# Optimization experiments

Measured on AMD Instinct MI355X. Metric: run time of the kernel, lower is better.

## Reference

```python
import jax, jax.numpy as jnp
import numpy as np

LAYER_BS = 63
N_SITES = 12
B = 2048


def _kaiming_uniform(key, shape, fan_in):
    # torch kaiming_uniform_ with a=0: bound = sqrt(6/fan_in)
    bound = np.sqrt(6.0 / fan_in)
    return jax.random.uniform(key, shape, jnp.float32, -bound, bound)


def _cnn12(x, w):
    # x: (B, L, 12, Cin); w: (L, 3*Cin, Cout)
    nn0 = jnp.roll(x, -1, axis=-2) + jnp.roll(x, 3, axis=-2)
    nnn0 = jnp.roll(x, -2, axis=-2) + jnp.roll(x, 4, axis=-2)
    c0 = jnp.concatenate([nn0, nnn0], axis=-1)          # (B,L,12,2*Cin)
    c1 = c0 + jnp.roll(c0, -2, axis=-2)
    allc = jnp.concatenate([x, c1], axis=-1)            # (B,L,12,3*Cin)
    return jnp.einsum('blsc,lco->blso', allc, w)


def _batch_linear(x, w, b):
    # x: (B, L, F); w: (L, F, O); b: (L, O)
    return jnp.einsum('blf,lfo->blo', x, w) + b


def setup_inputs() -> dict:
    key = jax.random.key(0)
    ks = jax.random.split(key, 9)
    zs = jax.random.normal(ks[0], (B, LAYER_BS, N_SITES, 2), jnp.float32)
    # CNN weights: (L, 3*Cin, Cout); kaiming fan_in = 3*Cin
    w1 = _kaiming_uniform(ks[1], (LAYER_BS, 6, 32), 6)
    w2 = _kaiming_uniform(ks[2], (LAYER_BS, 96, 64), 96)
    fw1 = _kaiming_uniform(ks[3], (LAYER_BS, 128, 64), 128)
    fb1 = jax.random.uniform(ks[4], (LAYER_BS, 64), jnp.float32, -1 / np.sqrt(128), 1 / np.sqrt(128))
    fw2 = _kaiming_uniform(ks[5], (LAYER_BS, 64, 64), 64)
    fb2 = jax.random.uniform(ks[6], (LAYER_BS, 64), jnp.float32, -1 / np.sqrt(64), 1 / np.sqrt(64))
    fw3 = _kaiming_uniform(ks[7], (LAYER_BS, 64, 1), 64)
    fb3 = jax.random.uniform(ks[8], (LAYER_BS, 1), jnp.float32, -1 / np.sqrt(64), 1 / np.sqrt(64))
    return {"zs": zs, "w1": w1, "w2": w2, "fw1": fw1, "fb1": fb1,
            "fw2": fw2, "fb2": fb2, "fw3": fw3, "fb3": fb3}


def reference(zs, w1, w2, fw1, fb1, fw2, fb2, fw3, fb3):
    h = jax.nn.relu(_cnn12(zs, w1))                     # (B,L,12,32)
    h = jax.nn.relu(_cnn12(h, w2))                      # (B,L,12,64)
    h = jnp.concatenate([h.mean(axis=-2), h.max(axis=-2)], axis=-1)
    h = jax.nn.relu(_batch_linear(h, fw1, fb1))
    h = jax.nn.relu(_batch_linear(h, fw2, fb2))
    out = _batch_linear(h, fw3, fb3)                    # (B,L,1)
    return out[..., 0]                                  # (B,L)
```

## Files before the change

kernel.cpp:

```cpp
#include <hip/hip_runtime.h>


#define LNUM 63
#define BT 16
#define NBT 128
#define WSL 19968

typedef __attribute__((ext_vector_type(8))) _Float16 half8;
typedef __attribute__((ext_vector_type(2))) _Float16 half2v;
typedef __attribute__((ext_vector_type(4))) float floatx4;
typedef __attribute__((ext_vector_type(4))) unsigned uint4v;

static __device__ __forceinline__ unsigned cvtpk(float a, float b) {
    return __builtin_bit_cast(unsigned, __builtin_amdgcn_cvt_pkrtz(a, b));
}
static __device__ __forceinline__ half2v u2h(unsigned u) { return __builtin_bit_cast(half2v, u); }
static __device__ __forceinline__ float hlo16(unsigned short s) {
    return (float)__builtin_bit_cast(_Float16, s);
}
static __device__ __forceinline__ int w12(int v) { return v >= 12 ? v - 12 : v; }
static __device__ __forceinline__ float2 add2(float2 a, float2 b) { return make_float2(a.x + b.x, a.y + b.y); }

#define O_POOLDW 3072
#define O_POOLUS 6144
#define O_POOL2  0
#define O_G2     1280

__global__ void prep(const float* __restrict__ w2, const float* __restrict__ fw1,
                     const float* __restrict__ fw2, unsigned short* __restrict__ ws) {
    __shared__ float S[8192];
    const int l = blockIdx.x, r = blockIdx.y, t = threadIdx.x;
    if (r == 0) {
        const float4* src = (const float4*)(w2 + (size_t)l * 6144);
        #pragma unroll
        for (int j = 0; j < 6; ++j) *(float4*)(S + 4 * (t + 256 * j)) = src[t + 256 * j];
        __syncthreads();
        unsigned* dst = (unsigned*)(ws + (size_t)l * WSL);
        #pragma unroll
        for (int j = 0; j < 13; ++j) {
            int i = j * 256 + t, o = i / 52, cp = i - 52 * o, c = 2 * cp;
            dst[i] = cvtpk(S[c * 64 + o], S[c * 64 + 64 + o]);
        }
    } else if (r == 1) {
        const float4* src = (const float4*)(fw1 + (size_t)l * 8192);
        #pragma unroll
        for (int j = 0; j < 8; ++j) *(float4*)(S + 4 * (t + 256 * j)) = src[t + 256 * j];
        __syncthreads();
        unsigned* dst = (unsigned*)(ws + (size_t)l * WSL + 6656);
        #pragma unroll
        for (int j = 0; j < 17; ++j) {
            int i = j * 256 + t, o = i / 68, cp = i - 68 * o;
            dst[i] = cvtpk(S[cp * 64 + o], S[(64 + cp) * 64 + o]);
        }
    } else {
        const float4* src = (const float4*)(fw2 + (size_t)l * 4096);
        #pragma unroll
        for (int j = 0; j < 4; ++j) *(float4*)(S + 4 * (t + 256 * j)) = src[t + 256 * j];
        __syncthreads();
        unsigned* dst = (unsigned*)(ws + (size_t)l * WSL + 15360);
        #pragma unroll
        for (int j = 0; j < 9; ++j) {
            int i = j * 256 + t, o = i / 36, cp = i - 36 * o, c = 2 * cp;
            dst[i] = cvtpk(S[c * 64 + o], S[c * 64 + 64 + o]);
        }
    }
}

__global__ __launch_bounds__(256, 4) void fused_nn(
    const float* __restrict__ zs,  const float* __restrict__ w1,
    const float* __restrict__ fb1, const float* __restrict__ fb2,
    const float* __restrict__ fw3, const float* __restrict__ fb3,
    const unsigned short* __restrict__ ws,
    float* __restrict__ out)
{
    __shared__ __align__(16) unsigned U[4160];
    unsigned short* USH = (unsigned short*)U;

    const int t    = threadIdx.x;
    const int lane = t & 63;
    const int wv   = t >> 6;
    const int n    = lane & 15;
    const int quad = lane >> 4;
    const int l    = blockIdx.x / NBT;
    const int b0   = (blockIdx.x % NBT) * BT;

    uint4v bwp[3][4];
    {
        const uint4v* w2q = (const uint4v*)(ws + (size_t)l * WSL);
        #pragma unroll
        for (int ks = 0; ks < 3; ++ks)
            #pragma unroll
            for (int nt = 0; nt < 4; ++nt)
                bwp[ks][nt] = w2q[(nt * 16 + n) * 13 + ks * 4 + quad];
    }

    {
        const int b = t >> 4, cpair = t & 15, c0 = cpair * 2;
        const float* xb = zs + ((size_t)(b0 + b) * LNUM + l) * 24;
        float4 xq[6];
        #pragma unroll
        for (int q = 0; q < 6; ++q) xq[q] = *(const float4*)(xb + q * 4);
        float2 xv[12], xr[12], xA[12], xB[12];
        #pragma unroll
        for (int s = 0; s < 12; ++s)
            xv[s] = (s & 1) ? make_float2(xq[s >> 1].z, xq[s >> 1].w)
                            : make_float2(xq[s >> 1].x, xq[s >> 1].y);
        #pragma unroll
        for (int s = 0; s < 12; ++s) xr[s] = add2(xv[w12(s + 1)], xv[w12(s + 11)]);
        #pragma unroll
        for (int s = 0; s < 12; ++s) {
            xA[s] = add2(xr[w12(s + 2)], xr[w12(s + 10)]);
            xB[s] = add2(xr[w12(s + 3)], xr[w12(s + 9)]);
        }
        const float* wl = w1 + (size_t)l * 192 + c0;
        const float2 w0  = *(const float2*)(wl);
        const float2 w1v = *(const float2*)(wl + 32);
        const float2 w2v = *(const float2*)(wl + 64);
        const float2 w3v = *(const float2*)(wl + 96);
        const float2 w4v = *(const float2*)(wl + 128);
        const float2 w5v = *(const float2*)(wl + 160);
        #pragma unroll
        for (int s = 0; s < 12; ++s) {
            float hx = xv[s].x*w0.x + xv[s].y*w1v.x + xA[s].x*w2v.x + xA[s].y*w3v.x
                     + xB[s].x*w4v.x + xB[s].y*w5v.x;
            float hy = xv[s].x*w0.y + xv[s].y*w1v.y + xA[s].x*w2v.y + xA[s].y*w3v.y
                     + xB[s].x*w4v.y + xB[s].y*w5v.y;
            U[(b * 12 + s) * 20 + cpair] = cvtpk(fmaxf(hx, 0.f), fmaxf(hy, 0.f));
        }
    }
    const float bias1 = fb1[(size_t)l * 64 + wv * 16 + n];
    const float bias2 = fb2[(size_t)l * 64 + wv * 16 + n];
    __syncthreads();

    floatx4 acc[3][4];
    #pragma unroll
    for (int mi = 0; mi < 3; ++mi)
        #pragma unroll
        for (int nt = 0; nt < 4; ++nt) acc[mi][nt] = (floatx4){0.f, 0.f, 0.f, 0.f};
    {
        int bi[3], si[3];
        #pragma unroll
        for (int mi = 0; mi < 3; ++mi) {
            int row = 48 * wv + 16 * mi + n;
            bi[mi] = row / 12;
            si[mi] = row - 12 * bi[mi];
        }
        const int q4 = quad * 4;
        const int dA[4] = {1, 11, 3, 9};
        const int dB[4] = {2, 10, 4, 8};
        #pragma unroll
        for (int ks = 0; ks < 3; ++ks) {
            half8 af[3];
            #pragma unroll
            for (int mi = 0; mi < 3; ++mi) {
                const int rb = bi[mi] * 12, s = si[mi];
                if (ks == 0) {
                    af[mi] = *(const half8*)(U + (rb + s) * 20 + q4);
                } else {
                    const int* d = (ks == 1) ? dA : dB;
                    half8 l0 = *(const half8*)(U + (rb + w12(s + d[0])) * 20 + q4);
                    half8 l1 = *(const half8*)(U + (rb + w12(s + d[1])) * 20 + q4);
                    half8 l2 = *(const half8*)(U + (rb + w12(s + d[2])) * 20 + q4);
                    half8 l3 = *(const half8*)(U + (rb + w12(s + d[3])) * 20 + q4);
                    af[mi] = (l0 + l1) + (l2 + l3);
                }
            }
            #pragma unroll
            for (int mi = 0; mi < 3; ++mi)
                #pragma unroll
                for (int nt = 0; nt < 4; ++nt)
                    acc[mi][nt] = __builtin_amdgcn_mfma_f32_16x16x32_f16(
                        af[mi], __builtin_bit_cast(half8, bwp[ks][nt]), acc[mi][nt], 0, 0, 0);
        }
    }
    __syncthreads();

    #pragma unroll
    for (int mi = 0; mi < 3; ++mi) {
        const int rr = 48 * wv + 16 * mi + 4 * quad;
        const int bq = rr / 12;
        const int chk = (rr - 12 * bq) >> 2;
        #pragma unroll
        for (int nt = 0; nt < 4; ++nt) {
            const int ch = nt * 16 + n;
            float r0 = fmaxf(acc[mi][nt][0], 0.f), r1 = fmaxf(acc[mi][nt][1], 0.f);
            float r2 = fmaxf(acc[mi][nt][2], 0.f), r3 = fmaxf(acc[mi][nt][3], 0.f);
            float sm = (r0 + r1) + (r2 + r3);
            float mx = fmaxf(fmaxf(r0, r1), fmaxf(r2, r3));
            U[(bq * 64 + ch) * 3 + chk] = cvtpk(sm, mx);
        }
    }
    __builtin_amdgcn_wave_barrier();

    {
        const unsigned* p = U + t * 12;
        uint4v q0 = *(const uint4v*)(p);
        uint4v q1 = *(const uint4v*)(p + 4);
        uint4v q2 = *(const uint4v*)(p + 8);
        unsigned arr[12] = {q0.x, q0.y, q0.z, q0.w, q1.x, q1.y, q1.z, q1.w,
                            q2.x, q2.y, q2.z, q2.w};
        const int b = t >> 4, ch0 = (t * 4) & 63;
        const _Float16 inv12 = (_Float16)(1.0f / 12.0f);
        unsigned pk[4];
        #pragma unroll
        for (int j = 0; j < 4; ++j) {
            half2v d0 = u2h(arr[3 * j]), d1 = u2h(arr[3 * j + 1]), d2 = u2h(arr[3 * j + 2]);
            _Float16 s = (d0[0] + d1[0]) + d2[0];
            _Float16 m0 = d0[1] > d1[1] ? d0[1] : d1[1];
            _Float16 m  = m0 > d2[1] ? m0 : d2[1];
            half2v pm;
            pm[0] = s * inv12;
            pm[1] = m;
            pk[j] = __builtin_bit_cast(unsigned, pm);
        }
        uint2 w01 = make_uint2(pk[0], pk[1]), w23 = make_uint2(pk[2], pk[3]);
        *(uint2*)(U + O_POOLDW + b * 68 + ch0)     = w01;
        *(uint2*)(U + O_POOLDW + b * 68 + ch0 + 2) = w23;
    }
    __syncthreads();

    {
        const int o = wv * 16 + n;
        floatx4 a1 = (floatx4){bias1, bias1, bias1, bias1};
        const uint4v* f1q = (const uint4v*)(ws + (size_t)l * WSL + 6656);
        #pragma unroll
        for (int ks = 0; ks < 4; ++ks) {
            half8 av = *(const half8*)(USH + O_POOLUS + n * 136 + ks * 32 + quad * 8);
            uint4v bw = f1q[o * 17 + ks * 4 + quad];
            a1 = __builtin_amdgcn_mfma_f32_16x16x32_f16(av, __builtin_bit_cast(half8, bw), a1, 0, 0, 0);
        }
        #pragma unroll
        for (int i = 0; i < 2; ++i) {
            unsigned pk = cvtpk(fmaxf(a1[2 * i], 0.f), fmaxf(a1[2 * i + 1], 0.f));
            USH[O_POOL2 + (quad * 4 + 2 * i)     * 72 + o] = (unsigned short)(pk & 0xffffu);
            USH[O_POOL2 + (quad * 4 + 2 * i + 1) * 72 + o] = (unsigned short)(pk >> 16);
        }
    }
    __syncthreads();

    {
        const int o = wv * 16 + n;
        floatx4 a2 = (floatx4){bias2, bias2, bias2, bias2};
        const uint4v* f2q = (const uint4v*)(ws + (size_t)l * WSL + 15360);
        #pragma unroll
        for (int ks = 0; ks < 2; ++ks) {
            half8 av = *(const half8*)(USH + O_POOL2 + n * 72 + ks * 32 + quad * 8);
            uint4v bw = f2q[o * 9 + ks * 4 + quad];
            a2 = __builtin_amdgcn_mfma_f32_16x16x32_f16(av, __builtin_bit_cast(half8, bw), a2, 0, 0, 0);
        }
        #pragma unroll
        for (int i = 0; i < 2; ++i) {
            unsigned pk = cvtpk(fmaxf(a2[2 * i], 0.f), fmaxf(a2[2 * i + 1], 0.f));
            USH[O_G2 + (quad * 4 + 2 * i)     * 72 + o] = (unsigned short)(pk & 0xffffu);
            USH[O_G2 + (quad * 4 + 2 * i + 1) * 72 + o] = (unsigned short)(pk >> 16);
        }
    }
    __syncthreads();

    if (t < 16) {
        float a = fb3[l];
        const float* w3 = fw3 + (size_t)l * 64;
        #pragma unroll
        for (int c4 = 0; c4 < 16; ++c4) {
            uint2 u2 = *(const uint2*)(USH + O_G2 + t * 72 + c4 * 4);
            float4 w = *(const float4*)(w3 + c4 * 4);
            a += hlo16((unsigned short)(u2.x & 0xffff)) * w.x
               + hlo16((unsigned short)(u2.x >> 16))    * w.y
               + hlo16((unsigned short)(u2.y & 0xffff)) * w.z
               + hlo16((unsigned short)(u2.y >> 16))    * w.w;
        }
        out[(size_t)(b0 + t) * LNUM + l] = a;
    }
}

extern "C" void kernel_launch(void* const* d_in, const int* in_sizes, int n_in,
                              void* d_out, int out_size, void* d_ws, size_t ws_size,
                              hipStream_t stream) {
    const float* zs  = (const float*)d_in[0];
    const float* w1  = (const float*)d_in[1];
    const float* w2  = (const float*)d_in[2];
    const float* fw1 = (const float*)d_in[3];
    const float* fb1 = (const float*)d_in[4];
    const float* fw2 = (const float*)d_in[5];
    const float* fb2 = (const float*)d_in[6];
    const float* fw3 = (const float*)d_in[7];
    const float* fb3 = (const float*)d_in[8];
    float* out = (float*)d_out;
    unsigned short* ws = (unsigned short*)d_ws;

    hipLaunchKernelGGL(prep, dim3(LNUM, 3), dim3(256), 0, stream, w2, fw1, fw2, ws);
    hipLaunchKernelGGL(fused_nn, dim3(LNUM * NBT), dim3(256), 0, stream,
                       zs, w1, fb1, fb2, fw3, fb3, ws, out);
}
```

Baseline: 133.7 us.

## Process two 16-batch tiles per block to amortize weight loads

Each block now handles 32 batch rows in two sequential 16-row tiles through the conv stages. The conv2 weight fragments held in registers and the per-layer biases are reused across both tiles, and the FC layers run two MFMA row tiles that share each weight fragment. Shared memory grows and the block count halves, which lowers occupancy and the number of blocks available for parallelism. Extra barriers were added before the FC output writes because the pooled buffer now overlaps the FC output regions.

Result: slower. 240.7 us (+80.1%).

```diff
diff --git a/kernel.cpp b/kernel.cpp
--- a/kernel.cpp
+++ b/kernel.cpp
@@ -2,8 +2,8 @@
 
 
 #define LNUM 63
-#define BT 16
-#define NBT 128
+#define BT 32
+#define NBT 64
 #define WSL 19968
 
 typedef __attribute__((ext_vector_type(8))) _Float16 half8;
@@ -21,10 +21,10 @@
 static __device__ __forceinline__ int w12(int v) { return v >= 12 ? v - 12 : v; }
 static __device__ __forceinline__ float2 add2(float2 a, float2 b) { return make_float2(a.x + b.x, a.y + b.y); }
 
-#define O_POOLDW 3072
-#define O_POOLUS 6144
+#define O_POOLDW 4096
+#define O_POOLUS 8192
 #define O_POOL2  0
-#define O_G2     1280
+#define O_G2     2304
 
 __global__ void prep(const float* __restrict__ w2, const float* __restrict__ fw1,
                      const float* __restrict__ fw2, unsigned short* __restrict__ ws) {
@@ -73,7 +73,7 @@
     const unsigned short* __restrict__ ws,
     float* __restrict__ out)
 {
-    __shared__ __align__(16) unsigned U[4160];
+    __shared__ __align__(16) unsigned U[6272];
     unsigned short* USH = (unsigned short*)U;
 
     const int t    = threadIdx.x;
@@ -93,171 +93,188 @@
             for (int nt = 0; nt < 4; ++nt)
                 bwp[ks][nt] = w2q[(nt * 16 + n) * 13 + ks * 4 + quad];
     }
-
-    {
-        const int b = t >> 4, cpair = t & 15, c0 = cpair * 2;
-        const float* xb = zs + ((size_t)(b0 + b) * LNUM + l) * 24;
-        float4 xq[6];
-        #pragma unroll
-        for (int q = 0; q < 6; ++q) xq[q] = *(const float4*)(xb + q * 4);
-        float2 xv[12], xr[12], xA[12], xB[12];
-        #pragma unroll
-        for (int s = 0; s < 12; ++s)
-            xv[s] = (s & 1) ? make_float2(xq[s >> 1].z, xq[s >> 1].w)
-                            : make_float2(xq[s >> 1].x, xq[s >> 1].y);
-        #pragma unroll
-        for (int s = 0; s < 12; ++s) xr[s] = add2(xv[w12(s + 1)], xv[w12(s + 11)]);
-        #pragma unroll
-        for (int s = 0; s < 12; ++s) {
-            xA[s] = add2(xr[w12(s + 2)], xr[w12(s + 10)]);
-            xB[s] = add2(xr[w12(s + 3)], xr[w12(s + 9)]);
-        }
-        const float* wl = w1 + (size_t)l * 192 + c0;
-        const float2 w0  = *(const float2*)(wl);
-        const float2 w1v = *(const float2*)(wl + 32);
-        const float2 w2v = *(const float2*)(wl + 64);
-        const float2 w3v = *(const float2*)(wl + 96);
-        const float2 w4v = *(const float2*)(wl + 128);
-        const float2 w5v = *(const float2*)(wl + 160);
-        #pragma unroll
-        for (int s = 0; s < 12; ++s) {
-            float hx = xv[s].x*w0.x + xv[s].y*w1v.x + xA[s].x*w2v.x + xA[s].y*w3v.x
-                     + xB[s].x*w4v.x + xB[s].y*w5v.x;
-            float hy = xv[s].x*w0.y + xv[s].y*w1v.y + xA[s].x*w2v.y + xA[s].y*w3v.y
-                     + xB[s].x*w4v.y + xB[s].y*w5v.y;
-            U[(b * 12 + s) * 20 + cpair] = cvtpk(fmaxf(hx, 0.f), fmaxf(hy, 0.f));
-        }
-    }
     const float bias1 = fb1[(size_t)l * 64 + wv * 16 + n];
     const float bias2 = fb2[(size_t)l * 64 + wv * 16 + n];
-    __syncthreads();
-
-    floatx4 acc[3][4];
-    #pragma unroll
-    for (int mi = 0; mi < 3; ++mi)
-        #pragma unroll
-        for (int nt = 0; nt < 4; ++nt) acc[mi][nt] = (floatx4){0.f, 0.f, 0.f, 0.f};
-    {
-        int bi[3], si[3];
+
+    for (int tile = 0; tile < 2; ++tile) {
+        const int bb0 = b0 + 16 * tile;
+
+        {
+            const int b = t >> 4, cpair = t & 15, c0 = cpair * 2;
+            const float* xb = zs + ((size_t)(bb0 + b) * LNUM + l) * 24;
+            float4 xq[6];
+            #pragma unroll
+            for (int q = 0; q < 6; ++q) xq[q] = *(const float4*)(xb + q * 4);
+            float2 xv[12], xr[12], xA[12], xB[12];
+            #pragma unroll
+            for (int s = 0; s < 12; ++s)
+                xv[s] = (s & 1) ? make_float2(xq[s >> 1].z, xq[s >> 1].w)
+                                : make_float2(xq[s >> 1].x, xq[s >> 1].y);
+            #pragma unroll
+            for (int s = 0; s < 12; ++s) xr[s] = add2(xv[w12(s + 1)], xv[w12(s + 11)]);
+            #pragma unroll
+            for (int s = 0; s < 12; ++s) {
+                xA[s] = add2(xr[w12(s + 2)], xr[w12(s + 10)]);
+                xB[s] = add2(xr[w12(s + 3)], xr[w12(s + 9)]);
+            }
+            const float* wl = w1 + (size_t)l * 192 + c0;
+            const float2 w0  = *(const float2*)(wl);
+            const float2 w1v = *(const float2*)(wl + 32);
+            const float2 w2v = *(const float2*)(wl + 64);
+            const float2 w3v = *(const float2*)(wl + 96);
+            const float2 w4v = *(const float2*)(wl + 128);
+            const float2 w5v = *(const float2*)(wl + 160);
+            #pragma unroll
+            for (int s = 0; s < 12; ++s) {
+                float hx = xv[s].x*w0.x + xv[s].y*w1v.x + xA[s].x*w2v.x + xA[s].y*w3v.x
+                         + xB[s].x*w4v.x + xB[s].y*w5v.x;
+                float hy = xv[s].x*w0.y + xv[s].y*w1v.y + xA[s].x*w2v.y + xA[s].y*w3v.y
+                         + xB[s].x*w4v.y + xB[s].y*w5v.y;
+                U[(b * 12 + s) * 20 + cpair] = cvtpk(fmaxf(hx, 0.f), fmaxf(hy, 0.f));
+            }
+        }
+        __syncthreads();
+
+        floatx4 acc[3][4];
+        #pragma unroll
+        for (int mi = 0; mi < 3; ++mi)
+            #pragma unroll
+            for (int nt = 0; nt < 4; ++nt) acc[mi][nt] = (floatx4){0.f, 0.f, 0.f, 0.f};
+        {
+            int bi[3], si[3];
+            #pragma unroll
+            for (int mi = 0; mi < 3; ++mi) {
+                int row = 48 * wv + 16 * mi + n;
+                bi[mi] = row / 12;
+                si[mi] = row - 12 * bi[mi];
+            }
+            const int q4 = quad * 4;
+            const int dA[4] = {1, 11, 3, 9};
+            const int dB[4] = {2, 10, 4, 8};
+            #pragma unroll
+            for (int ks = 0; ks < 3; ++ks) {
+                half8 af[3];
+                #pragma unroll
+                for (int mi = 0; mi < 3; ++mi) {
+                    const int rb = bi[mi] * 12, s = si[mi];
+                    if (ks == 0) {
+                        af[mi] = *(const half8*)(U + (rb + s) * 20 + q4);
+                    } else {
+                        const int* d = (ks == 1) ? dA : dB;
+                        half8 l0 = *(const half8*)(U + (rb + w12(s + d[0])) * 20 + q4);
+                        half8 l1 = *(const half8*)(U + (rb + w12(s + d[1])) * 20 + q4);
+                        half8 l2 = *(const half8*)(U + (rb + w12(s + d[2])) * 20 + q4);
+                        half8 l3 = *(const half8*)(U + (rb + w12(s + d[3])) * 20 + q4);
+                        af[mi] = (l0 + l1) + (l2 + l3);
+                    }
+                }
+                #pragma unroll
+                for (int mi = 0; mi < 3; ++mi)
+                    #pragma unroll
+                    for (int nt = 0; nt < 4; ++nt)
+                        acc[mi][nt] = __builtin_amdgcn_mfma_f32_16x16x32_f16(
+                            af[mi], __builtin_bit_cast(half8, bwp[ks][nt]), acc[mi][nt], 0, 0, 0);
+            }
+        }
+        __syncthreads();
+
         #pragma unroll
         for (int mi = 0; mi < 3; ++mi) {
-            int row = 48 * wv + 16 * mi + n;
-            bi[mi] = row / 12;
-            si[mi] = row - 12 * bi[mi];
-        }
-        const int q4 = quad * 4;
-        const int dA[4] = {1, 11, 3, 9};
-        const int dB[4] = {2, 10, 4, 8};
-        #pragma unroll
-        for (int ks = 0; ks < 3; ++ks) {
-            half8 af[3];
-            #pragma unroll
-            for (int mi = 0; mi < 3; ++mi) {
-                const int rb = bi[mi] * 12, s = si[mi];
-                if (ks == 0) {
-                    af[mi] = *(const half8*)(U + (rb + s) * 20 + q4);
-                } else {
-                    const int* d = (ks == 1) ? dA : dB;
-                    half8 l0 = *(const half8*)(U + (rb + w12(s + d[0])) * 20 + q4);
-                    half8 l1 = *(const half8*)(U + (rb + w12(s + d[1])) * 20 + q4);
-                    half8 l2 = *(const half8*)(U + (rb + w12(s + d[2])) * 20 + q4);
-                    half8 l3 = *(const half8*)(U + (rb + w12(s + d[3])) * 20 + q4);
-                    af[mi] = (l0 + l1) + (l2 + l3);
-                }
-            }
-            #pragma unroll
-            for (int mi = 0; mi < 3; ++mi)
-                #pragma unroll
-                for (int nt = 0; nt < 4; ++nt)
-                    acc[mi][nt] = __builtin_amdgcn_mfma_f32_16x16x32_f16(
-                        af[mi], __builtin_bit_cast(half8, bwp[ks][nt]), acc[mi][nt], 0, 0, 0);
-        }
-    }
-    __syncthreads();
-
-    #pragma unroll
-    for (int mi = 0; mi < 3; ++mi) {
-        const int rr = 48 * wv + 16 * mi + 4 * quad;
-        const int bq = rr / 12;
-        const int chk = (rr - 12 * bq) >> 2;
-        #pragma unroll
-        for (int nt = 0; nt < 4; ++nt) {
-            const int ch = nt * 16 + n;
-            float r0 = fmaxf(acc[mi][nt][0], 0.f), r1 = fmaxf(acc[mi][nt][1], 0.f);
-            float r2 = fmaxf(acc[mi][nt][2], 0.f), r3 = fmaxf(acc[mi][nt][3], 0.f);
-            float sm = (r0 + r1) + (r2 + r3);
-            float mx = fmaxf(fmaxf(r0, r1), fmaxf(r2, r3));
-            U[(bq * 64 + ch) * 3 + chk] = cvtpk(sm, mx);
-        }
-    }
-    __builtin_amdgcn_wave_barrier();
-
-    {
-        const unsigned* p = U + t * 12;
-        uint4v q0 = *(const uint4v*)(p);
-        uint4v q1 = *(const uint4v*)(p + 4);
-        uint4v q2 = *(const uint4v*)(p + 8);
-        unsigned arr[12] = {q0.x, q0.y, q0.z, q0.w, q1.x, q1.y, q1.z, q1.w,
-                            q2.x, q2.y, q2.z, q2.w};
-        const int b = t >> 4, ch0 = (t * 4) & 63;
-        const _Float16 inv12 = (_Float16)(1.0f / 12.0f);
-        unsigned pk[4];
-        #pragma unroll
-        for (int j = 0; j < 4; ++j) {
-            half2v d0 = u2h(arr[3 * j]), d1 = u2h(arr[3 * j + 1]), d2 = u2h(arr[3 * j + 2]);
-            _Float16 s = (d0[0] + d1[0]) + d2[0];
-            _Float16 m0 = d0[1] > d1[1] ? d0[1] : d1[1];
-            _Float16 m  = m0 > d2[1] ? m0 : d2[1];
-            half2v pm;
-            pm[0] = s * inv12;
-            pm[1] = m;
-            pk[j] = __builtin_bit_cast(unsigned, pm);
-        }
-        uint2 w01 = make_uint2(pk[0], pk[1]), w23 = make_uint2(pk[2], pk[3]);
-        *(uint2*)(U + O_POOLDW + b * 68 + ch0)     = w01;
-        *(uint2*)(U + O_POOLDW + b * 68 + ch0 + 2) = w23;
-    }
-    __syncthreads();
+            const int rr = 48 * wv + 16 * mi + 4 * quad;
+            const int bq = rr / 12;
+            const int chk = (rr - 12 * bq) >> 2;
+            #pragma unroll
+            for (int nt = 0; nt < 4; ++nt) {
+                const int ch = nt * 16 + n;
+                float r0 = fmaxf(acc[mi][nt][0], 0.f), r1 = fmaxf(acc[mi][nt][1], 0.f);
+                float r2 = fmaxf(acc[mi][nt][2], 0.f), r3 = fmaxf(acc[mi][nt][3], 0.f);
+                float sm = (r0 + r1) + (r2 + r3);
+                float mx = fmaxf(fmaxf(r0, r1), fmaxf(r2, r3));
+                U[(bq * 64 + ch) * 3 + chk] = cvtpk(sm, mx);
+            }
+        }
+        __builtin_amdgcn_wave_barrier();
+
+        {
+            const unsigned* p = U + t * 12;
+            uint4v q0 = *(const uint4v*)(p);
+            uint4v q1 = *(const uint4v*)(p + 4);
+            uint4v q2 = *(const uint4v*)(p + 8);
+            unsigned arr[12] = {q0.x, q0.y, q0.z, q0.w, q1.x, q1.y, q1.z, q1.w,
+                                q2.x, q2.y, q2.z, q2.w};
+            const int b = t >> 4, ch0 = (t * 4) & 63;
+            const _Float16 inv12 = (_Float16)(1.0f / 12.0f);
+            unsigned pk[4];
+            #pragma unroll
+            for (int j = 0; j < 4; ++j) {
+                half2v d0 = u2h(arr[3 * j]), d1 = u2h(arr[3 * j + 1]), d2 = u2h(arr[3 * j + 2]);
+                _Float16 s = (d0[0] + d1[0]) + d2[0];
+                _Float16 m0 = d0[1] > d1[1] ? d0[1] : d1[1];
+                _Float16 m  = m0 > d2[1] ? m0 : d2[1];
+                half2v pm;
+                pm[0] = s * inv12;
+                pm[1] = m;
+                pk[j] = __builtin_bit_cast(unsigned, pm);
+            }
+            uint2 w01 = make_uint2(pk[0], pk[1]), w23 = make_uint2(pk[2], pk[3]);
+            const int prow = tile * 16 + b;
+            *(uint2*)(U + O_POOLDW + prow * 68 + ch0)     = w01;
+            *(uint2*)(U + O_POOLDW + prow * 68 + ch0 + 2) = w23;
+        }
+        __syncthreads();
+    }
 
     {
         const int o = wv * 16 + n;
-        floatx4 a1 = (floatx4){bias1, bias1, bias1, bias1};
+        floatx4 a1[2] = {(floatx4){bias1, bias1, bias1, bias1},
+                         (floatx4){bias1, bias1, bias1, bias1}};
         const uint4v* f1q = (const uint4v*)(ws + (size_t)l * WSL + 6656);
         #pragma unroll
         for (int ks = 0; ks < 4; ++ks) {
-            half8 av = *(const half8*)(USH + O_POOLUS + n * 136 + ks * 32 + quad * 8);
-            uint4v bw = f1q[o * 17 + ks * 4 + quad];
-            a1 = __builtin_amdgcn_mfma_f32_16x16x32_f16(av, __builtin_bit_cast(half8, bw), a1, 0, 0, 0);
-        }
-        #pragma unroll
-        for (int i = 0; i < 2; ++i) {
-            unsigned pk = cvtpk(fmaxf(a1[2 * i], 0.f), fmaxf(a1[2 * i + 1], 0.f));
-            USH[O_POOL2 + (quad * 4 + 2 * i)     * 72 + o] = (unsigned short)(pk & 0xffffu);
-            USH[O_POOL2 + (quad * 4 + 2 * i + 1) * 72 + o] = (unsigned short)(pk >> 16);
-        }
+            half8 av0 = *(const half8*)(USH + O_POOLUS + n * 136 + ks * 32 + quad * 8);
+            half8 av1 = *(const half8*)(USH + O_POOLUS + (16 + n) * 136 + ks * 32 + quad * 8);
+            half8 bw = __builtin_bit_cast(half8, f1q[o * 17 + ks * 4 + quad]);
+            a1[0] = __builtin_amdgcn_mfma_f32_16x16x32_f16(av0, bw, a1[0], 0, 0, 0);
+            a1[1] = __builtin_amdgcn_mfma_f32_16x16x32_f16(av1, bw, a1[1], 0, 0, 0);
+        }
+        __syncthreads();
+        #pragma unroll
+        for (int j = 0; j < 2; ++j)
+            #pragma unroll
+            for (int i = 0; i < 2; ++i) {
+                unsigned pk = cvtpk(fmaxf(a1[j][2 * i], 0.f), fmaxf(a1[j][2 * i + 1], 0.f));
+                USH[O_POOL2 + (j * 16 + quad * 4 + 2 * i)     * 72 + o] = (unsigned short)(pk & 0xffffu);
+                USH[O_POOL2 + (j * 16 + quad * 4 + 2 * i + 1) * 72 + o] = (unsigned short)(pk >> 16);
+            }
     }
     __syncthreads();
 
     {
         const int o = wv * 16 + n;
-        floatx4 a2 = (floatx4){bias2, bias2, bias2, bias2};
+        floatx4 a2[2] = {(floatx4){bias2, bias2, bias2, bias2},
+                         (floatx4){bias2, bias2, bias2, bias2}};
         const uint4v* f2q = (const uint4v*)(ws + (size_t)l * WSL + 15360);
         #pragma unroll
         for (int ks = 0; ks < 2; ++ks) {
-            half8 av = *(const half8*)(USH + O_POOL2 + n * 72 + ks * 32 + quad * 8);
-            uint4v bw = f2q[o * 9 + ks * 4 + quad];
-            a2 = __builtin_amdgcn_mfma_f32_16x16x32_f16(av, __builtin_bit_cast(half8, bw), a2, 0, 0, 0);
-        }
-        #pragma unroll
-        for (int i = 0; i < 2; ++i) {
-            unsigned pk = cvtpk(fmaxf(a2[2 * i], 0.f), fmaxf(a2[2 * i + 1], 0.f));
-            USH[O_G2 + (quad * 4 + 2 * i)     * 72 + o] = (unsigned short)(pk & 0xffffu);
-            USH[O_G2 + (quad * 4 + 2 * i + 1) * 72 + o] = (unsigned short)(pk >> 16);
-        }
+            half8 av0 = *(const half8*)(USH + O_POOL2 + n * 72 + ks * 32 + quad * 8);
+            half8 av1 = *(const half8*)(USH + O_POOL2 + (16 + n) * 72 + ks * 32 + quad * 8);
+            half8 bw = __builtin_bit_cast(half8, f2q[o * 9 + ks * 4 + quad]);
+            a2[0] = __builtin_amdgcn_mfma_f32_16x16x32_f16(av0, bw, a2[0], 0, 0, 0);
+            a2[1] = __builtin_amdgcn_mfma_f32_16x16x32_f16(av1, bw, a2[1], 0, 0, 0);
+        }
+        __syncthreads();
+        #pragma unroll
+        for (int j = 0; j < 2; ++j)
+            #pragma unroll
+            for (int i = 0; i < 2; ++i) {
+                unsigned pk = cvtpk(fmaxf(a2[j][2 * i], 0.f), fmaxf(a2[j][2 * i + 1], 0.f));
+                USH[O_G2 + (j * 16 + quad * 4 + 2 * i)     * 72 + o] = (unsigned short)(pk & 0xffffu);
+                USH[O_G2 + (j * 16 + quad * 4 + 2 * i + 1) * 72 + o] = (unsigned short)(pk >> 16);
+            }
     }
     __syncthreads();
 
-    if (t < 16) {
+    if (t < BT) {
         float a = fb3[l];
         const float* w3 = fw3 + (size_t)l * 64;
         #pragma unroll
```
